# Optimization experiments

Hardware: AMD Instinct MI355X
Metric: run time of the kernel (lower is better)

Reference implementation:

```python
import jax, jax.numpy as jnp
import numpy as np

N, D, K = 65536, 1024, 256

def setup_inputs() -> dict:
    key = jax.random.key(0)
    k1, k2 = jax.random.split(key)
    inputs = jax.random.normal(k1, (N, D), dtype=jnp.float32)
    centroids = jax.random.normal(k2, (K, D), dtype=jnp.float32)
    return {"inputs": inputs, "centroids": centroids}

def reference(inputs, centroids):
    # Squared euclidean distances [K, N] without materializing [K, N, D]:
    # ||c||^2 + ||x||^2 - 2 c @ x^T  (same math as sum(square(x[None]-c[:,None]), -1))
    x_sq = jnp.sum(inputs * inputs, axis=1)            # [N]
    c_sq = jnp.sum(centroids * centroids, axis=1)      # [K]
    cross = jnp.einsum('kd,nd->kn', centroids, inputs) # [K, N]
    distances = c_sq[:, None] + x_sq[None, :] - 2.0 * cross  # [K, N]
    assignments = jnp.argmin(distances, axis=0)        # [N], int
    # calculate_loss: sum_c mean(where(assign==c, distances, 0)) over the full
    # [K,N] grid. Since each n matches exactly one cluster c, the per-cluster
    # masked means sum to the global mean of distances.
    loss = jnp.mean(distances)
    return distances, assignments, loss
```

## Files before the change

### kernel.cpp

```cpp
#include <hip/hip_runtime.h>
#include <cstdint>

#define N_PTS 65536
#define DIM   1024
#define K_CL  256
#define BN    256
#define BK    32
#define NT    (DIM / BK)
#define THREADS 512

typedef __bf16 bf16_t;
typedef bf16_t bf16x8 __attribute__((ext_vector_type(8)));
typedef float  f32x4  __attribute__((ext_vector_type(4)));

union U16x8 { uint4 u4; bf16x8 bf; ushort us[8]; };

__device__ __forceinline__ ushort f2bf_rne(float f) {
    uint32_t u = __float_as_uint(f);
    uint32_t r = (u + 0x7FFFu + ((u >> 16) & 1u)) >> 16;
    return (ushort)r;
}
__device__ __forceinline__ float bf2f(ushort b) {
    return __uint_as_float(((uint32_t)b) << 16);
}

__device__ __forceinline__ void gll16(const void* g, void* l) {
    __builtin_amdgcn_global_load_lds(
        (const __attribute__((address_space(1))) void*)g,
        (__attribute__((address_space(3))) void*)l, 16, 0, 0);
}

__global__ __launch_bounds__(128) void km_prep(const float* __restrict__ cent,
                                               ushort* __restrict__ Ahi,
                                               ushort* __restrict__ Alo,
                                               float* __restrict__ csq) {
    const int r  = blockIdx.x;
    const int j  = threadIdx.x;
    const int kt = j >> 2;
    const int gp = j & 3;
    const int s  = (r >> 1) & 3;
    const int d0 = kt * BK + ((gp ^ s) << 3);

    const float* src = cent + r * DIM + d0;
    float4 a = *(const float4*)src;
    float4 b = *(const float4*)(src + 4);
    float v[8] = {a.x, a.y, a.z, a.w, b.x, b.y, b.z, b.w};

    U16x8 hi, lo;
    float ss = 0.f;
#pragma unroll
    for (int i = 0; i < 8; ++i) {
        float f = v[i];
        ss += f * f;
        ushort h = f2bf_rne(f);
        hi.us[i] = h;
        lo.us[i] = f2bf_rne(f - bf2f(h));
    }
    *(uint4*)(Ahi + kt * (K_CL * BK) + r * BK + gp * 8) = hi.u4;
    *(uint4*)(Alo + kt * (K_CL * BK) + r * BK + gp * 8) = lo.u4;

#pragma unroll
    for (int off = 1; off < 64; off <<= 1) ss += __shfl_xor(ss, off);
    __shared__ float ws2[2];
    if ((j & 63) == 0) ws2[j >> 6] = ss;
    __syncthreads();
    if (j == 0) csq[r] = ws2[0] + ws2[1];
}

__global__ __launch_bounds__(THREADS, 2) void km_main(
    const float* __restrict__ x,
    const ushort* __restrict__ Ahi, const ushort* __restrict__ Alo,
    const float* __restrict__ csq,
    float* __restrict__ out_dist, float* __restrict__ out_assign,
    float* __restrict__ partials) {

    __shared__ __align__(16) ushort sAhi[2][K_CL * BK];
    __shared__ __align__(16) ushort sAlo[2][K_CL * BK];
    __shared__ __align__(16) ushort sBhi[2][BN * BK];
    __shared__ __align__(16) ushort sBlo[2][BN * BK];
    __shared__ __align__(16) float  sCsq[K_CL];
    __shared__ __align__(16) float  sXsq[BN];
    __shared__ float sRedV[4 * BN];
    __shared__ int   sRedI[4 * BN];
    __shared__ float sWsum[8];

    const int tid  = threadIdx.x;
    const int blk  = blockIdx.x;
    const int lane = tid & 63;
    const int w    = tid >> 6;
    const int wr   = w >> 1;
    const int wc   = w & 1;
    const int l15  = lane & 15;
    const int l4   = lane >> 4;

    if (tid < K_CL) sCsq[tid] = csq[tid];

    const int bcol  = tid >> 1;
    const int bhalf = tid & 1;
    const int bs    = (bcol >> 1) & 3;
    const int bOff0 = bcol * BK + ((((bhalf << 1) | 0) ^ bs) << 3);
    const int bOff1 = bcol * BK + ((((bhalf << 1) | 1) ^ bs) << 3);
    const float* xsrc = x + (size_t)(blk * BN + bcol) * DIM + bhalf * 16;

    float xs_acc = 0.f;

    auto stageA = [&](int kt, int buf) {
        const char* ph = (const char*)Ahi + kt * 16384 + tid * 16;
        const char* pl = (const char*)Alo + kt * 16384 + tid * 16;
        char* dh = (char*)&sAhi[buf][0] + tid * 16;
        char* dl = (char*)&sAlo[buf][0] + tid * 16;
        gll16(ph, dh);
        gll16(ph + 8192, dh + 8192);
        gll16(pl, dl);
        gll16(pl + 8192, dl + 8192);
    };
    auto writeB = [&](int buf, float4 v0, float4 v1, float4 v2, float4 v3) {
        float f[16] = {v0.x, v0.y, v0.z, v0.w, v1.x, v1.y, v1.z, v1.w,
                       v2.x, v2.y, v2.z, v2.w, v3.x, v3.y, v3.z, v3.w};
        U16x8 h0, h1, l0, l1;
#pragma unroll
        for (int i = 0; i < 8; ++i) {
            float a = f[i];
            xs_acc += a * a;
            ushort h = f2bf_rne(a);
            h0.us[i] = h;
            l0.us[i] = f2bf_rne(a - bf2f(h));
            float b = f[i + 8];
            xs_acc += b * b;
            ushort hb = f2bf_rne(b);
            h1.us[i] = hb;
            l1.us[i] = f2bf_rne(b - bf2f(hb));
        }
        *(uint4*)&sBhi[buf][bOff0] = h0.u4;
        *(uint4*)&sBhi[buf][bOff1] = h1.u4;
        *(uint4*)&sBlo[buf][bOff0] = l0.u4;
        *(uint4*)&sBlo[buf][bOff1] = l1.u4;
    };

    int aOff[4], bOff[8];
#pragma unroll
    for (int f = 0; f < 4; ++f) {
        int row  = wr * 64 + f * 16 + l15;
        aOff[f]  = row * BK + ((l4 ^ ((row >> 1) & 3)) << 3);
    }
#pragma unroll
    for (int f = 0; f < 8; ++f) {
        int col  = wc * 128 + f * 16 + l15;
        bOff[f]  = col * BK + ((l4 ^ ((col >> 1) & 3)) << 3);
    }

    float4 b0, b1, b2, b3;
    stageA(0, 0);
    b0 = *(const float4*)(xsrc);
    b1 = *(const float4*)(xsrc + 4);
    b2 = *(const float4*)(xsrc + 8);
    b3 = *(const float4*)(xsrc + 12);
    writeB(0, b0, b1, b2, b3);
    __syncthreads();

    f32x4 acc[4][8];
#pragma unroll
    for (int i = 0; i < 4; ++i)
#pragma unroll
        for (int q = 0; q < 8; ++q) acc[i][q] = (f32x4){0.f, 0.f, 0.f, 0.f};

    for (int kt = 0; kt < NT; ++kt) {
        const int cur = kt & 1, nxt = cur ^ 1;
        if (kt + 1 < NT) {
            stageA(kt + 1, nxt);
            const float* p = xsrc + (kt + 1) * BK;
            b0 = *(const float4*)p;
            b1 = *(const float4*)(p + 4);
            b2 = *(const float4*)(p + 8);
            b3 = *(const float4*)(p + 12);
        }
        U16x8 ah[4], al[4];
#pragma unroll
        for (int f = 0; f < 4; ++f) {
            ah[f].u4 = *(const uint4*)&sAhi[cur][aOff[f]];
            al[f].u4 = *(const uint4*)&sAlo[cur][aOff[f]];
        }
#pragma unroll
        for (int fj = 0; fj < 8; ++fj) {
            U16x8 bh, bl;
            bh.u4 = *(const uint4*)&sBhi[cur][bOff[fj]];
            bl.u4 = *(const uint4*)&sBlo[cur][bOff[fj]];
#pragma unroll
            for (int fi = 0; fi < 4; ++fi) {
                acc[fi][fj] = __builtin_amdgcn_mfma_f32_16x16x32_bf16(ah[fi].bf, bh.bf, acc[fi][fj], 0, 0, 0);
                acc[fi][fj] = __builtin_amdgcn_mfma_f32_16x16x32_bf16(ah[fi].bf, bl.bf, acc[fi][fj], 0, 0, 0);
                acc[fi][fj] = __builtin_amdgcn_mfma_f32_16x16x32_bf16(al[fi].bf, bh.bf, acc[fi][fj], 0, 0, 0);
            }
        }
        if (kt + 1 < NT) writeB(nxt, b0, b1, b2, b3);
        __syncthreads();
    }

    {
        float v = xs_acc;
        v += __shfl_xor(v, 1);
        if (bhalf == 0) sXsq[bcol] = v;
    }
    __syncthreads();

    const int colBase = wc * 128;
    float xs[8];
    f32x4 cs[4];
#pragma unroll
    for (int f = 0; f < 8; ++f) xs[f] = sXsq[colBase + f * 16 + l15];
#pragma unroll
    for (int f = 0; f < 4; ++f) cs[f] = *(const f32x4*)&sCsq[wr * 64 + f * 16 + l4 * 4];

    float lsum = 0.f;
    float bestv[8];
    int   bestr[8];
#pragma unroll
    for (int f = 0; f < 8; ++f) { bestv[f] = 3.4e38f; bestr[f] = 0; }

#pragma unroll
    for (int fi = 0; fi < 4; ++fi) {
        const int rowB = wr * 64 + fi * 16 + l4 * 4;
#pragma unroll
        for (int fj = 0; fj < 8; ++fj) {
            const int col = blk * BN + colBase + fj * 16 + l15;
            float* outp = out_dist + (size_t)rowB * N_PTS + col;
#pragma unroll
            for (int j = 0; j < 4; ++j) {
                float d = cs[fi][j] + xs[fj] - 2.0f * acc[fi][fj][j];
                outp[(size_t)j * N_PTS] = d;
                lsum += d;
                int r = rowB + j;
                if (d < bestv[fj]) { bestv[fj] = d; bestr[fj] = r; }
            }
        }
    }

#pragma unroll
    for (int fj = 0; fj < 8; ++fj) {
#pragma unroll
        for (int m = 16; m <= 32; m <<= 1) {
            float ov = __shfl_xor(bestv[fj], m);
            int   orr = __shfl_xor(bestr[fj], m);
            if (ov < bestv[fj] || (ov == bestv[fj] && orr < bestr[fj])) {
                bestv[fj] = ov; bestr[fj] = orr;
            }
        }
        if (lane < 16) {
            sRedV[wr * BN + colBase + fj * 16 + lane] = bestv[fj];
            sRedI[wr * BN + colBase + fj * 16 + lane] = bestr[fj];
        }
    }

#pragma unroll
    for (int off = 1; off < 64; off <<= 1) lsum += __shfl_xor(lsum, off);
    if (lane == 0) sWsum[w] = lsum;
    __syncthreads();

    if (tid < BN) {
        float bv = sRedV[tid];
        int   br = sRedI[tid];
#pragma unroll
        for (int q = 1; q < 4; ++q) {
            float v = sRedV[q * BN + tid];
            int   r = sRedI[q * BN + tid];
            if (v < bv || (v == bv && r < br)) { bv = v; br = r; }
        }
        out_assign[blk * BN + tid] = (float)br;
    }
    if (tid == 0) {
        float t = 0.f;
#pragma unroll
        for (int q = 0; q < 8; ++q) t += sWsum[q];
        partials[blk] = t;
    }
}

__global__ __launch_bounds__(256) void km_fin(const float* __restrict__ partials,
                                              float* __restrict__ out_loss) {
    __shared__ float ws[4];
    const int t = threadIdx.x;
    float v = partials[t];
#pragma unroll
    for (int off = 1; off < 64; off <<= 1) v += __shfl_xor(v, off);
    if ((t & 63) == 0) ws[t >> 6] = v;
    __syncthreads();
    if (t == 0) {
        float s = 0.f;
#pragma unroll
        for (int i = 0; i < 4; ++i) s += ws[i];
        out_loss[0] = s / 16777216.0f;
    }
}

extern "C" void kernel_launch(void* const* d_in, const int* in_sizes, int n_in,
                              void* d_out, int out_size, void* d_ws, size_t ws_size,
                              hipStream_t stream) {
    const float* x    = (const float*)d_in[0];
    const float* cent = (const float*)d_in[1];

    float* out        = (float*)d_out;
    float* out_dist   = out;
    float* out_assign = out + (size_t)K_CL * N_PTS;
    float* out_loss   = out_assign + N_PTS;

    char*   ws       = (char*)d_ws;
    float*  csq      = (float*)ws;
    float*  partials = (float*)(ws + 1024);
    ushort* Ahi      = (ushort*)(ws + 4096);
    ushort* Alo      = (ushort*)(ws + 4096 + 524288);

    km_prep<<<dim3(K_CL), dim3(128), 0, stream>>>(cent, Ahi, Alo, csq);
    km_main<<<dim3(N_PTS / BN), dim3(THREADS), 0, stream>>>(
        x, Ahi, Alo, csq, out_dist, out_assign, partials);
    km_fin<<<dim3(1), dim3(256), 0, stream>>>(partials, out_loss);
}
```

Before: 143.7 us.

## Interleave LDS reads, async loads and MFMA clusters with explicit barriers and priorities

Splits each K-tile iteration into four phases. In each phase the wave issues LDS reads for two B fragments, interleaved with split hi/lo global-to-LDS prefetches of A and the B conversion and write. It then synchronizes with s_barrier and explicit waitcnt, and runs an MFMA cluster at raised s_setprio. The goal is to overlap memory traffic with tensor-core work and to keep waves in lockstep, in the style of ping-pong scheduling. It also replaces the manual bf16 rounding with native bf16 casts and uses fma for the squared norm. The extra barriers and hand-placed vmcnt waits add sync overhead and carry correctness risk if the wait counts are wrong.

Result: faster. 121.8 us (-15.2%).

```diff
diff --git a/kernel.cpp b/kernel.cpp
--- a/kernel.cpp
+++ b/kernel.cpp
@@ -29,6 +29,12 @@
         (const __attribute__((address_space(1))) void*)g,
         (__attribute__((address_space(3))) void*)l, 16, 0, 0);
 }
+
+#define BAR()   __builtin_amdgcn_s_barrier()
+#define LGKM0() do { asm volatile("s_waitcnt lgkmcnt(0)" ::: "memory"); \
+                     __builtin_amdgcn_sched_barrier(0); } while (0)
+#define VMCNT(N) do { asm volatile("s_waitcnt vmcnt(" #N ")" ::: "memory"); \
+                      __builtin_amdgcn_sched_barrier(0); } while (0)
 
 __global__ __launch_bounds__(128) void km_prep(const float* __restrict__ cent,
                                                ushort* __restrict__ Ahi,
@@ -104,13 +110,15 @@
 
     float xs_acc = 0.f;
 
-    auto stageA = [&](int kt, int buf) {
+    auto stageA_hi = [&](int kt, int buf) {
         const char* ph = (const char*)Ahi + kt * 16384 + tid * 16;
-        const char* pl = (const char*)Alo + kt * 16384 + tid * 16;
         char* dh = (char*)&sAhi[buf][0] + tid * 16;
-        char* dl = (char*)&sAlo[buf][0] + tid * 16;
         gll16(ph, dh);
         gll16(ph + 8192, dh + 8192);
+    };
+    auto stageA_lo = [&](int kt, int buf) {
+        const char* pl = (const char*)Alo + kt * 16384 + tid * 16;
+        char* dl = (char*)&sAlo[buf][0] + tid * 16;
         gll16(pl, dl);
         gll16(pl + 8192, dl + 8192);
     };
@@ -121,15 +129,15 @@
 #pragma unroll
         for (int i = 0; i < 8; ++i) {
             float a = f[i];
-            xs_acc += a * a;
-            ushort h = f2bf_rne(a);
-            h0.us[i] = h;
-            l0.us[i] = f2bf_rne(a - bf2f(h));
+            xs_acc = fmaf(a, a, xs_acc);
+            bf16_t hb = (bf16_t)a;
+            h0.bf[i] = hb;
+            l0.bf[i] = (bf16_t)(a - (float)hb);
             float b = f[i + 8];
-            xs_acc += b * b;
-            ushort hb = f2bf_rne(b);
-            h1.us[i] = hb;
-            l1.us[i] = f2bf_rne(b - bf2f(hb));
+            xs_acc = fmaf(b, b, xs_acc);
+            bf16_t hc = (bf16_t)b;
+            h1.bf[i] = hc;
+            l1.bf[i] = (bf16_t)(b - (float)hc);
         }
         *(uint4*)&sBhi[buf][bOff0] = h0.u4;
         *(uint4*)&sBhi[buf][bOff1] = h1.u4;
@@ -150,7 +158,8 @@
     }
 
     float4 b0, b1, b2, b3;
-    stageA(0, 0);
+    stageA_hi(0, 0);
+    stageA_lo(0, 0);
     b0 = *(const float4*)(xsrc);
     b1 = *(const float4*)(xsrc + 4);
     b2 = *(const float4*)(xsrc + 8);
@@ -164,37 +173,86 @@
 #pragma unroll
         for (int q = 0; q < 8; ++q) acc[i][q] = (f32x4){0.f, 0.f, 0.f, 0.f};
 
+#define MFMA_PAIR(FJ)                                                                                  \
+    _Pragma("unroll")                                                                                  \
+    for (int fi = 0; fi < 4; ++fi) {                                                                   \
+        acc[fi][FJ]     = __builtin_amdgcn_mfma_f32_16x16x32_bf16(ah[fi].bf, bhx.bf, acc[fi][FJ], 0, 0, 0);     \
+        acc[fi][FJ]     = __builtin_amdgcn_mfma_f32_16x16x32_bf16(ah[fi].bf, blx.bf, acc[fi][FJ], 0, 0, 0);     \
+        acc[fi][FJ]     = __builtin_amdgcn_mfma_f32_16x16x32_bf16(al[fi].bf, bhx.bf, acc[fi][FJ], 0, 0, 0);     \
+        acc[fi][FJ + 1] = __builtin_amdgcn_mfma_f32_16x16x32_bf16(ah[fi].bf, bhy.bf, acc[fi][FJ + 1], 0, 0, 0); \
+        acc[fi][FJ + 1] = __builtin_amdgcn_mfma_f32_16x16x32_bf16(ah[fi].bf, bly.bf, acc[fi][FJ + 1], 0, 0, 0); \
+        acc[fi][FJ + 1] = __builtin_amdgcn_mfma_f32_16x16x32_bf16(al[fi].bf, bhy.bf, acc[fi][FJ + 1], 0, 0, 0); \
+    }
+
+#define DS_READ_PAIR(FJ)                                  \
+    bhx.u4 = *(const uint4*)&sBhi[cur][bOff[FJ]];         \
+    blx.u4 = *(const uint4*)&sBlo[cur][bOff[FJ]];         \
+    bhy.u4 = *(const uint4*)&sBhi[cur][bOff[(FJ) + 1]];   \
+    bly.u4 = *(const uint4*)&sBlo[cur][bOff[(FJ) + 1]];
+
     for (int kt = 0; kt < NT; ++kt) {
-        const int cur = kt & 1, nxt = cur ^ 1;
-        if (kt + 1 < NT) {
-            stageA(kt + 1, nxt);
+        const int  cur = kt & 1, nxt = cur ^ 1;
+        const bool pf  = (kt + 1 < NT);
+
+        U16x8 ah[4], al[4], bhx, blx, bhy, bly;
+
+        if (pf) {
             const float* p = xsrc + (kt + 1) * BK;
             b0 = *(const float4*)p;
             b1 = *(const float4*)(p + 4);
             b2 = *(const float4*)(p + 8);
             b3 = *(const float4*)(p + 12);
         }
-        U16x8 ah[4], al[4];
 #pragma unroll
         for (int f = 0; f < 4; ++f) {
             ah[f].u4 = *(const uint4*)&sAhi[cur][aOff[f]];
             al[f].u4 = *(const uint4*)&sAlo[cur][aOff[f]];
         }
-#pragma unroll
-        for (int fj = 0; fj < 8; ++fj) {
-            U16x8 bh, bl;
-            bh.u4 = *(const uint4*)&sBhi[cur][bOff[fj]];
-            bl.u4 = *(const uint4*)&sBlo[cur][bOff[fj]];
-#pragma unroll
-            for (int fi = 0; fi < 4; ++fi) {
-                acc[fi][fj] = __builtin_amdgcn_mfma_f32_16x16x32_bf16(ah[fi].bf, bh.bf, acc[fi][fj], 0, 0, 0);
-                acc[fi][fj] = __builtin_amdgcn_mfma_f32_16x16x32_bf16(ah[fi].bf, bl.bf, acc[fi][fj], 0, 0, 0);
-                acc[fi][fj] = __builtin_amdgcn_mfma_f32_16x16x32_bf16(al[fi].bf, bh.bf, acc[fi][fj], 0, 0, 0);
-            }
-        }
-        if (kt + 1 < NT) writeB(nxt, b0, b1, b2, b3);
-        __syncthreads();
-    }
+        DS_READ_PAIR(0)
+        if (pf) stageA_hi(kt + 1, nxt);
+        __builtin_amdgcn_sched_barrier(0);
+        BAR();
+        LGKM0();
+        __builtin_amdgcn_s_setprio(1);
+        MFMA_PAIR(0)
+        __builtin_amdgcn_s_setprio(0);
+        BAR();
+
+        DS_READ_PAIR(2)
+        if (pf) stageA_lo(kt + 1, nxt);
+        __builtin_amdgcn_sched_barrier(0);
+        BAR();
+        LGKM0();
+        __builtin_amdgcn_s_setprio(1);
+        MFMA_PAIR(2)
+        __builtin_amdgcn_s_setprio(0);
+        BAR();
+
+        DS_READ_PAIR(4)
+        __builtin_amdgcn_sched_barrier(0);
+        BAR();
+        LGKM0();
+        __builtin_amdgcn_s_setprio(1);
+        MFMA_PAIR(4)
+        __builtin_amdgcn_s_setprio(0);
+        BAR();
+
+        DS_READ_PAIR(6)
+        if (pf) {
+            VMCNT(4);
+            writeB(nxt, b0, b1, b2, b3);
+        }
+        __builtin_amdgcn_sched_barrier(0);
+        BAR();
+        LGKM0();
+        __builtin_amdgcn_s_setprio(1);
+        MFMA_PAIR(6)
+        __builtin_amdgcn_s_setprio(0);
+        if (pf) VMCNT(0);
+        BAR();
+    }
+#undef MFMA_PAIR
+#undef DS_READ_PAIR
 
     {
         float v = xs_acc;
```

## Halve column tile, single-buffer A, prefetch B two steps ahead with explicit waits

Applied to the files above, without the earlier changes.

Shrinks the per-block column tile from 256 to 128 points with 256 threads, so each of four waves owns 64 centroid rows across all 128 columns and the grid doubles to 512 blocks. The A (centroid) tile becomes single-buffered: fragments are read into registers first, then a barrier frees the buffer for the next async global-to-LDS load. The x tile is now prefetched two k-steps ahead, with explicit vmcnt/lgkmcnt waits, sched barriers and raised wave priority around the MFMA block to overlap loads with compute. It also swaps the manual bf16 rounding for native casts and resizes the final reduction to 512 partials; the extra barrier per step and the hand-tuned wait counts add synchronization cost and a risk of ordering mistakes.

Result: faster. 118.0 us, median of 3 (-17.9%).

```diff
diff --git a/kernel.cpp b/kernel.cpp
--- a/kernel.cpp
+++ b/kernel.cpp
@@ -4,10 +4,10 @@
 #define N_PTS 65536
 #define DIM   1024
 #define K_CL  256
-#define BN    256
+#define BN    128
 #define BK    32
 #define NT    (DIM / BK)
-#define THREADS 512
+#define THREADS 256
 
 typedef __bf16 bf16_t;
 typedef bf16_t bf16x8 __attribute__((ext_vector_type(8)));
@@ -29,6 +29,14 @@
         (const __attribute__((address_space(1))) void*)g,
         (__attribute__((address_space(3))) void*)l, 16, 0, 0);
 }
+
+#define BAR()   __builtin_amdgcn_s_barrier()
+#define SCHB()  __builtin_amdgcn_sched_barrier(0)
+#define LGKM0() do { asm volatile("s_waitcnt lgkmcnt(0)" ::: "memory"); \
+                     __builtin_amdgcn_sched_barrier(0); } while (0)
+#define VMCNT(N) do { asm volatile("s_waitcnt vmcnt(" #N ")" ::: "memory"); \
+                      __builtin_amdgcn_sched_barrier(0); } while (0)
+#define MFMA(ACC, A, B) (ACC) = __builtin_amdgcn_mfma_f32_16x16x32_bf16((A).bf, (B).bf, (ACC), 0, 0, 0)
 
 __global__ __launch_bounds__(128) void km_prep(const float* __restrict__ cent,
                                                ushort* __restrict__ Ahi,
@@ -74,26 +82,24 @@
     float* __restrict__ out_dist, float* __restrict__ out_assign,
     float* __restrict__ partials) {
 
-    __shared__ __align__(16) ushort sAhi[2][K_CL * BK];
-    __shared__ __align__(16) ushort sAlo[2][K_CL * BK];
+    __shared__ __align__(16) ushort sAhi[K_CL * BK];
+    __shared__ __align__(16) ushort sAlo[K_CL * BK];
     __shared__ __align__(16) ushort sBhi[2][BN * BK];
     __shared__ __align__(16) ushort sBlo[2][BN * BK];
     __shared__ __align__(16) float  sCsq[K_CL];
     __shared__ __align__(16) float  sXsq[BN];
     __shared__ float sRedV[4 * BN];
     __shared__ int   sRedI[4 * BN];
-    __shared__ float sWsum[8];
+    __shared__ float sWsum[4];
 
     const int tid  = threadIdx.x;
     const int blk  = blockIdx.x;
     const int lane = tid & 63;
     const int w    = tid >> 6;
-    const int wr   = w >> 1;
-    const int wc   = w & 1;
     const int l15  = lane & 15;
     const int l4   = lane >> 4;
 
-    if (tid < K_CL) sCsq[tid] = csq[tid];
+    sCsq[tid] = csq[tid];
 
     const int bcol  = tid >> 1;
     const int bhalf = tid & 1;
@@ -104,15 +110,19 @@
 
     float xs_acc = 0.f;
 
-    auto stageA = [&](int kt, int buf) {
+    auto stageA = [&](int kt) {
         const char* ph = (const char*)Ahi + kt * 16384 + tid * 16;
         const char* pl = (const char*)Alo + kt * 16384 + tid * 16;
-        char* dh = (char*)&sAhi[buf][0] + tid * 16;
-        char* dl = (char*)&sAlo[buf][0] + tid * 16;
-        gll16(ph, dh);
-        gll16(ph + 8192, dh + 8192);
-        gll16(pl, dl);
-        gll16(pl + 8192, dl + 8192);
+        char* dh = (char*)&sAhi[0] + tid * 16;
+        char* dl = (char*)&sAlo[0] + tid * 16;
+        gll16(ph,         dh);
+        gll16(ph +  4096, dh +  4096);
+        gll16(ph +  8192, dh +  8192);
+        gll16(ph + 12288, dh + 12288);
+        gll16(pl,         dl);
+        gll16(pl +  4096, dl +  4096);
+        gll16(pl +  8192, dl +  8192);
+        gll16(pl + 12288, dl + 12288);
     };
     auto writeB = [&](int buf, float4 v0, float4 v1, float4 v2, float4 v3) {
         float f[16] = {v0.x, v0.y, v0.z, v0.w, v1.x, v1.y, v1.z, v1.w,
@@ -121,15 +131,15 @@
 #pragma unroll
         for (int i = 0; i < 8; ++i) {
             float a = f[i];
-            xs_acc += a * a;
-            ushort h = f2bf_rne(a);
-            h0.us[i] = h;
-            l0.us[i] = f2bf_rne(a - bf2f(h));
+            xs_acc = fmaf(a, a, xs_acc);
+            bf16_t hb = (bf16_t)a;
+            h0.bf[i] = hb;
+            l0.bf[i] = (bf16_t)(a - (float)hb);
             float b = f[i + 8];
-            xs_acc += b * b;
-            ushort hb = f2bf_rne(b);
-            h1.us[i] = hb;
-            l1.us[i] = f2bf_rne(b - bf2f(hb));
+            xs_acc = fmaf(b, b, xs_acc);
+            bf16_t hc = (bf16_t)b;
+            h1.bf[i] = hc;
+            l1.bf[i] = (bf16_t)(b - (float)hc);
         }
         *(uint4*)&sBhi[buf][bOff0] = h0.u4;
         *(uint4*)&sBhi[buf][bOff1] = h1.u4;
@@ -140,22 +150,29 @@
     int aOff[4], bOff[8];
 #pragma unroll
     for (int f = 0; f < 4; ++f) {
-        int row  = wr * 64 + f * 16 + l15;
+        int row  = w * 64 + f * 16 + l15;
         aOff[f]  = row * BK + ((l4 ^ ((row >> 1) & 3)) << 3);
     }
 #pragma unroll
     for (int f = 0; f < 8; ++f) {
-        int col  = wc * 128 + f * 16 + l15;
+        int col  = f * 16 + l15;
         bOff[f]  = col * BK + ((l4 ^ ((col >> 1) & 3)) << 3);
     }
 
     float4 b0, b1, b2, b3;
-    stageA(0, 0);
+    stageA(0);
     b0 = *(const float4*)(xsrc);
     b1 = *(const float4*)(xsrc + 4);
     b2 = *(const float4*)(xsrc + 8);
     b3 = *(const float4*)(xsrc + 12);
     writeB(0, b0, b1, b2, b3);
+    {
+        const float* p = xsrc + BK;
+        b0 = *(const float4*)p;
+        b1 = *(const float4*)(p + 4);
+        b2 = *(const float4*)(p + 8);
+        b3 = *(const float4*)(p + 12);
+    }
     __syncthreads();
 
     f32x4 acc[4][8];
@@ -165,35 +182,47 @@
         for (int q = 0; q < 8; ++q) acc[i][q] = (f32x4){0.f, 0.f, 0.f, 0.f};
 
     for (int kt = 0; kt < NT; ++kt) {
-        const int cur = kt & 1, nxt = cur ^ 1;
-        if (kt + 1 < NT) {
-            stageA(kt + 1, nxt);
-            const float* p = xsrc + (kt + 1) * BK;
+        const int  cur = kt & 1, nxt = cur ^ 1;
+        const bool pf1 = (kt + 1 < NT);
+        const bool pf2 = (kt + 2 < NT);
+
+        U16x8 ah[4], al[4];
+#pragma unroll
+        for (int f = 0; f < 4; ++f) {
+            ah[f].u4 = *(const uint4*)&sAhi[aOff[f]];
+            al[f].u4 = *(const uint4*)&sAlo[aOff[f]];
+        }
+        LGKM0();
+        BAR();
+
+        if (pf1) stageA(kt + 1);
+        SCHB();
+        if (pf1) writeB(nxt, b0, b1, b2, b3);
+        if (pf2) {
+            const float* p = xsrc + (kt + 2) * BK;
             b0 = *(const float4*)p;
             b1 = *(const float4*)(p + 4);
             b2 = *(const float4*)(p + 8);
             b3 = *(const float4*)(p + 12);
         }
-        U16x8 ah[4], al[4];
-#pragma unroll
-        for (int f = 0; f < 4; ++f) {
-            ah[f].u4 = *(const uint4*)&sAhi[cur][aOff[f]];
-            al[f].u4 = *(const uint4*)&sAlo[cur][aOff[f]];
-        }
+        __builtin_amdgcn_s_setprio(1);
 #pragma unroll
         for (int fj = 0; fj < 8; ++fj) {
             U16x8 bh, bl;
             bh.u4 = *(const uint4*)&sBhi[cur][bOff[fj]];
             bl.u4 = *(const uint4*)&sBlo[cur][bOff[fj]];
 #pragma unroll
-            for (int fi = 0; fi < 4; ++fi) {
-                acc[fi][fj] = __builtin_amdgcn_mfma_f32_16x16x32_bf16(ah[fi].bf, bh.bf, acc[fi][fj], 0, 0, 0);
-                acc[fi][fj] = __builtin_amdgcn_mfma_f32_16x16x32_bf16(ah[fi].bf, bl.bf, acc[fi][fj], 0, 0, 0);
-                acc[fi][fj] = __builtin_amdgcn_mfma_f32_16x16x32_bf16(al[fi].bf, bh.bf, acc[fi][fj], 0, 0, 0);
-            }
-        }
-        if (kt + 1 < NT) writeB(nxt, b0, b1, b2, b3);
-        __syncthreads();
+            for (int fi = 0; fi < 4; ++fi) MFMA(acc[fi][fj], ah[fi], bh);
+#pragma unroll
+            for (int fi = 0; fi < 4; ++fi) MFMA(acc[fi][fj], ah[fi], bl);
+#pragma unroll
+            for (int fi = 0; fi < 4; ++fi) MFMA(acc[fi][fj], al[fi], bh);
+        }
+        __builtin_amdgcn_s_setprio(0);
+        if (pf2) { VMCNT(4); }
+        else     { VMCNT(0); }
+        LGKM0();
+        BAR();
     }
 
     {
@@ -203,13 +232,12 @@
     }
     __syncthreads();
 
-    const int colBase = wc * 128;
     float xs[8];
     f32x4 cs[4];
 #pragma unroll
-    for (int f = 0; f < 8; ++f) xs[f] = sXsq[colBase + f * 16 + l15];
-#pragma unroll
-    for (int f = 0; f < 4; ++f) cs[f] = *(const f32x4*)&sCsq[wr * 64 + f * 16 + l4 * 4];
+    for (int f = 0; f < 8; ++f) xs[f] = sXsq[f * 16 + l15];
+#pragma unroll
+    for (int f = 0; f < 4; ++f) cs[f] = *(const f32x4*)&sCsq[w * 64 + f * 16 + l4 * 4];
 
     float lsum = 0.f;
     float bestv[8];
@@ -219,10 +247,10 @@
 
 #pragma unroll
     for (int fi = 0; fi < 4; ++fi) {
-        const int rowB = wr * 64 + fi * 16 + l4 * 4;
+        const int rowB = w * 64 + fi * 16 + l4 * 4;
 #pragma unroll
         for (int fj = 0; fj < 8; ++fj) {
-            const int col = blk * BN + colBase + fj * 16 + l15;
+            const int col = blk * BN + fj * 16 + l15;
             float* outp = out_dist + (size_t)rowB * N_PTS + col;
 #pragma unroll
             for (int j = 0; j < 4; ++j) {
@@ -246,8 +274,8 @@
             }
         }
         if (lane < 16) {
-            sRedV[wr * BN + colBase + fj * 16 + lane] = bestv[fj];
-            sRedI[wr * BN + colBase + fj * 16 + lane] = bestr[fj];
+            sRedV[w * BN + fj * 16 + lane] = bestv[fj];
+            sRedI[w * BN + fj * 16 + lane] = bestr[fj];
         }
     }
 
@@ -270,14 +298,14 @@
     if (tid == 0) {
         float t = 0.f;
 #pragma unroll
-        for (int q = 0; q < 8; ++q) t += sWsum[q];
+        for (int q = 0; q < 4; ++q) t += sWsum[q];
         partials[blk] = t;
     }
 }
 
-__global__ __launch_bounds__(256) void km_fin(const float* __restrict__ partials,
+__global__ __launch_bounds__(512) void km_fin(const float* __restrict__ partials,
                                               float* __restrict__ out_loss) {
-    __shared__ float ws[4];
+    __shared__ float ws[8];
     const int t = threadIdx.x;
     float v = partials[t];
 #pragma unroll
@@ -287,7 +315,7 @@
     if (t == 0) {
         float s = 0.f;
 #pragma unroll
-        for (int i = 0; i < 4; ++i) s += ws[i];
+        for (int i = 0; i < 8; ++i) s += ws[i];
         out_loss[0] = s / 16777216.0f;
     }
 }
@@ -312,5 +340,5 @@
     km_prep<<<dim3(K_CL), dim3(128), 0, stream>>>(cent, Ahi, Alo, csq);
     km_main<<<dim3(N_PTS / BN), dim3(THREADS), 0, stream>>>(
         x, Ahi, Alo, csq, out_dist, out_assign, partials);
-    km_fin<<<dim3(1), dim3(256), 0, stream>>>(partials, out_loss);
-}
+    km_fin<<<dim3(1), dim3(512), 0, stream>>>(partials, out_loss);
+}
```

## Deepen x prefetch to two tiles and reorder main loop for MFMA overlap

Applied to the files above, without the earlier changes.

Restructures the K-loop so global loads of x run two tiles ahead. The B-tile conversion and LDS write now happen before the MFMA block instead of after it. MFMAs are regrouped so that independent accumulators are interleaved, and the MFMA section gets raised wave priority. Explicit vmcnt/lgkmcnt waits and sched barriers replace __syncthreads, and bf16 conversion now uses native casts. The aim is to hide global-load and conversion latency behind matrix math, at the cost of more live registers and hand-tuned wait counts that could be wrong.

Result: faster. 118.3 us (-17.7%).

```diff
diff --git a/kernel.cpp b/kernel.cpp
--- a/kernel.cpp
+++ b/kernel.cpp
@@ -29,6 +29,14 @@
         (const __attribute__((address_space(1))) void*)g,
         (__attribute__((address_space(3))) void*)l, 16, 0, 0);
 }
+
+#define BAR()   __builtin_amdgcn_s_barrier()
+#define SCHB()  __builtin_amdgcn_sched_barrier(0)
+#define LGKM0() do { asm volatile("s_waitcnt lgkmcnt(0)" ::: "memory"); \
+                     __builtin_amdgcn_sched_barrier(0); } while (0)
+#define VMCNT(N) do { asm volatile("s_waitcnt vmcnt(" #N ")" ::: "memory"); \
+                      __builtin_amdgcn_sched_barrier(0); } while (0)
+#define MFMA(ACC, A, B) (ACC) = __builtin_amdgcn_mfma_f32_16x16x32_bf16((A).bf, (B).bf, (ACC), 0, 0, 0)
 
 __global__ __launch_bounds__(128) void km_prep(const float* __restrict__ cent,
                                                ushort* __restrict__ Ahi,
@@ -109,9 +117,9 @@
         const char* pl = (const char*)Alo + kt * 16384 + tid * 16;
         char* dh = (char*)&sAhi[buf][0] + tid * 16;
         char* dl = (char*)&sAlo[buf][0] + tid * 16;
-        gll16(ph, dh);
+        gll16(ph,        dh);
         gll16(ph + 8192, dh + 8192);
-        gll16(pl, dl);
+        gll16(pl,        dl);
         gll16(pl + 8192, dl + 8192);
     };
     auto writeB = [&](int buf, float4 v0, float4 v1, float4 v2, float4 v3) {
@@ -121,15 +129,15 @@
 #pragma unroll
         for (int i = 0; i < 8; ++i) {
             float a = f[i];
-            xs_acc += a * a;
-            ushort h = f2bf_rne(a);
-            h0.us[i] = h;
-            l0.us[i] = f2bf_rne(a - bf2f(h));
+            xs_acc = fmaf(a, a, xs_acc);
+            bf16_t hb = (bf16_t)a;
+            h0.bf[i] = hb;
+            l0.bf[i] = (bf16_t)(a - (float)hb);
             float b = f[i + 8];
-            xs_acc += b * b;
-            ushort hb = f2bf_rne(b);
-            h1.us[i] = hb;
-            l1.us[i] = f2bf_rne(b - bf2f(hb));
+            xs_acc = fmaf(b, b, xs_acc);
+            bf16_t hc = (bf16_t)b;
+            h1.bf[i] = hc;
+            l1.bf[i] = (bf16_t)(b - (float)hc);
         }
         *(uint4*)&sBhi[buf][bOff0] = h0.u4;
         *(uint4*)&sBhi[buf][bOff1] = h1.u4;
@@ -156,6 +164,13 @@
     b2 = *(const float4*)(xsrc + 8);
     b3 = *(const float4*)(xsrc + 12);
     writeB(0, b0, b1, b2, b3);
+    {
+        const float* p = xsrc + BK;
+        b0 = *(const float4*)p;
+        b1 = *(const float4*)(p + 4);
+        b2 = *(const float4*)(p + 8);
+        b3 = *(const float4*)(p + 12);
+    }
     __syncthreads();
 
     f32x4 acc[4][8];
@@ -165,35 +180,49 @@
         for (int q = 0; q < 8; ++q) acc[i][q] = (f32x4){0.f, 0.f, 0.f, 0.f};
 
     for (int kt = 0; kt < NT; ++kt) {
-        const int cur = kt & 1, nxt = cur ^ 1;
-        if (kt + 1 < NT) {
-            stageA(kt + 1, nxt);
-            const float* p = xsrc + (kt + 1) * BK;
+        const int  cur = kt & 1, nxt = cur ^ 1;
+        const bool pf1 = (kt + 1 < NT);
+        const bool pf2 = (kt + 2 < NT);
+
+        U16x8 ah[4], al[4];
+#pragma unroll
+        for (int f = 0; f < 4; ++f) {
+            ah[f].u4 = *(const uint4*)&sAhi[cur][aOff[f]];
+            al[f].u4 = *(const uint4*)&sAlo[cur][aOff[f]];
+        }
+
+        if (pf1) stageA(kt + 1, nxt);
+        SCHB();
+        if (pf1) writeB(nxt, b0, b1, b2, b3);
+        SCHB();
+        if (pf2) {
+            const float* p = xsrc + (kt + 2) * BK;
             b0 = *(const float4*)p;
             b1 = *(const float4*)(p + 4);
             b2 = *(const float4*)(p + 8);
             b3 = *(const float4*)(p + 12);
         }
-        U16x8 ah[4], al[4];
-#pragma unroll
-        for (int f = 0; f < 4; ++f) {
-            ah[f].u4 = *(const uint4*)&sAhi[cur][aOff[f]];
-            al[f].u4 = *(const uint4*)&sAlo[cur][aOff[f]];
-        }
+        SCHB();
+
+        __builtin_amdgcn_s_setprio(1);
 #pragma unroll
         for (int fj = 0; fj < 8; ++fj) {
             U16x8 bh, bl;
             bh.u4 = *(const uint4*)&sBhi[cur][bOff[fj]];
             bl.u4 = *(const uint4*)&sBlo[cur][bOff[fj]];
 #pragma unroll
-            for (int fi = 0; fi < 4; ++fi) {
-                acc[fi][fj] = __builtin_amdgcn_mfma_f32_16x16x32_bf16(ah[fi].bf, bh.bf, acc[fi][fj], 0, 0, 0);
-                acc[fi][fj] = __builtin_amdgcn_mfma_f32_16x16x32_bf16(ah[fi].bf, bl.bf, acc[fi][fj], 0, 0, 0);
-                acc[fi][fj] = __builtin_amdgcn_mfma_f32_16x16x32_bf16(al[fi].bf, bh.bf, acc[fi][fj], 0, 0, 0);
-            }
-        }
-        if (kt + 1 < NT) writeB(nxt, b0, b1, b2, b3);
-        __syncthreads();
+            for (int fi = 0; fi < 4; ++fi) MFMA(acc[fi][fj], ah[fi], bh);
+#pragma unroll
+            for (int fi = 0; fi < 4; ++fi) MFMA(acc[fi][fj], ah[fi], bl);
+#pragma unroll
+            for (int fi = 0; fi < 4; ++fi) MFMA(acc[fi][fj], al[fi], bh);
+        }
+        __builtin_amdgcn_s_setprio(0);
+
+        if (pf2)      { VMCNT(4); }
+        else if (pf1) { VMCNT(0); }
+        LGKM0();
+        BAR();
     }
 
     {
```
